# Kernel tuning notes

Measured on AMD Instinct MI355X. Metric: run time of the kernel, lower is better.

## Reference

```python
import jax, jax.numpy as jnp
import numpy as np

N = 100000      # nodes
E = 1600000     # edges (avg degree 16)
D = 64          # in_channels == conv widths == lin width
G = 64          # graphs in batch
OUT = 10        # out_channels


def setup_inputs() -> dict:
    key = jax.random.key(0)
    ks = jax.random.split(key, 20)
    s = 0.1
    inp = {
        "x": jax.random.normal(ks[0], (N, D), jnp.float32),
        "edge_index": jax.random.randint(ks[1], (2, E), 0, N, dtype=jnp.int64),
        "batch": jnp.sort(jax.random.randint(ks[2], (N,), 0, G, dtype=jnp.int64)),
    }
    k = 3
    for i in range(3):  # 3 SAGEConv layers: lin_l (Wl, bl) on aggregated, lin_r (Wr, no bias) on root
        inp[f"c{i}_Wl"] = jax.random.normal(ks[k], (D, D), jnp.float32) * s; k += 1
        inp[f"c{i}_bl"] = jnp.zeros((D,), jnp.float32)
        inp[f"c{i}_Wr"] = jax.random.normal(ks[k], (D, D), jnp.float32) * s; k += 1
    inp["l0_W"] = jax.random.normal(ks[k], (D, D), jnp.float32) * s; k += 1
    inp["l0_b"] = jnp.zeros((D,), jnp.float32)
    inp["out_W"] = jax.random.normal(ks[k], (D, OUT), jnp.float32) * s; k += 1
    inp["out_b"] = jnp.zeros((OUT,), jnp.float32)
    return inp


def reference(x, edge_index, batch,
              c0_Wl, c0_bl, c0_Wr,
              c1_Wl, c1_bl, c1_Wr,
              c2_Wl, c2_bl, c2_Wr,
              l0_W, l0_b, out_W, out_b):
    src, dst = edge_index[0], edge_index[1]
    # in-degree of each target node (mean conv aggregation), computed once
    deg = jax.ops.segment_sum(jnp.ones((E,), x.dtype), dst, num_segments=N)
    inv_deg = (1.0 / jnp.maximum(deg, 1.0))[:, None]

    def sage(h, Wl, bl, Wr):
        # gather source features, mean-aggregate at targets, then lin_l(agg) + lin_r(h)
        agg = jax.ops.segment_sum(h[src], dst, num_segments=N) * inv_deg
        return agg @ Wl + bl + h @ Wr

    h = jax.nn.relu(sage(x, c0_Wl, c0_bl, c0_Wr))
    h = jax.nn.relu(sage(h, c1_Wl, c1_bl, c1_Wr))
    h = jax.nn.relu(sage(h, c2_Wl, c2_bl, c2_Wr))

    # global mean pool over graphs
    cnt = jax.ops.segment_sum(jnp.ones((N,), h.dtype), batch, num_segments=G)
    g = jax.ops.segment_sum(h, batch, num_segments=G) / jnp.maximum(cnt, 1.0)[:, None]

    g = jax.nn.relu(g @ l0_W + l0_b)
    return g @ out_W + out_b  # [G, OUT]
```

## Files before the change

### kernel.cpp

```cpp
#include <hip/hip_runtime.h>
#include <hip/hip_fp16.h>

#define WPB 8
#define PADK 136
#define BSH 8
#define BNODES 256
#define SC_BLOCKS 256
#define HIST_BLOCKS 256

typedef _Float16 half8 __attribute__((ext_vector_type(8)));
typedef float floatx4 __attribute__((ext_vector_type(4)));

#define TS16(v) (((((v)[0] + (v)[1]) + ((v)[2] + (v)[3])) + (((v)[4] + (v)[5]) + ((v)[6] + (v)[7]))) + \
                 ((((v)[8] + (v)[9]) + ((v)[10] + (v)[11])) + (((v)[12] + (v)[13]) + ((v)[14] + (v)[15]))))

__global__ __launch_bounds__(256) void gnn_pre(const int* __restrict__ dst,
                                               int* __restrict__ bkt_cnt, int nbkt, int E,
                                               const int* __restrict__ batch,
                                               float* __restrict__ gcnt, int N,
                                               const float4* __restrict__ xin,
                                               ushort4* __restrict__ x16o, int n4,
                                               __half* __restrict__ x16,
                                               __half* __restrict__ hA,
                                               __half* __restrict__ hB) {
    int tid = threadIdx.x;
    if (blockIdx.x < HIST_BLOCKS) {
        __shared__ int h[512];
        __shared__ int gb[64];
        for (int i = tid; i < nbkt; i += 256) h[i] = 0;
        if (tid < 64) gb[tid] = 0;
        __syncthreads();
        const int stride = HIST_BLOCKS * 256;
        for (int e = blockIdx.x * 256 + tid; e < E; e += stride)
            atomicAdd(&h[dst[e] >> BSH], 1);
        for (int i = blockIdx.x * 256 + tid; i < N; i += stride)
            atomicAdd(&gb[batch[i]], 1);
        __syncthreads();
        for (int i = tid; i < nbkt; i += 256) {
            int v = h[i];
            if (v) atomicAdd(&bkt_cnt[i], v);
        }
        if (tid < 64) {
            int v = gb[tid];
            if (v) atomicAdd(&gcnt[tid], (float)v);
        }
        if (blockIdx.x == 0 && tid < 64) {
            x16[(size_t)N * 64 + tid] = __ushort_as_half((unsigned short)0);
            hA[(size_t)N * 64 + tid] = __ushort_as_half((unsigned short)0);
            hB[(size_t)N * 64 + tid] = __ushort_as_half((unsigned short)0);
        }
    } else {
        int i = (blockIdx.x - HIST_BLOCKS) * 256 + tid;
        if (i < n4) {
            float4 f = xin[i];
            ushort4 o;
            o.x = __half_as_ushort(__float2half(f.x));
            o.y = __half_as_ushort(__float2half(f.y));
            o.z = __half_as_ushort(__float2half(f.z));
            o.w = __half_as_ushort(__float2half(f.w));
            x16o[i] = o;
        }
    }
}

__global__ void gnn_bkt_scan(const int* __restrict__ bkt_cnt, int* __restrict__ bkt_base,
                             int* __restrict__ bkt_cur, int* __restrict__ row_ptr,
                             int nbkt, int N) {
    int lane = threadIdx.x;
    int carry = 0;
    for (int base = 0; base < nbkt; base += 64) {
        int idx = base + lane;
        int v = (idx < nbkt) ? bkt_cnt[idx] : 0;
        int x = v;
#pragma unroll
        for (int off = 1; off < 64; off <<= 1) {
            int y = __shfl_up(x, off);
            if (lane >= off) x += y;
        }
        if (idx < nbkt) {
            bkt_base[idx] = carry + (x - v);
            bkt_cur[idx] = carry + (x - v);
        }
        carry += __shfl(x, 63);
    }
    if (lane == 0) {
        bkt_base[nbkt] = carry;
        row_ptr[N] = carry;
    }
}

__global__ __launch_bounds__(256) void gnn_bkt_scatter(const int* __restrict__ src,
                                                       const int* __restrict__ dst,
                                                       int* __restrict__ bkt_cur,
                                                       unsigned int* __restrict__ pairs,
                                                       int E, int nbkt) {
    __shared__ int hist[512];
    __shared__ int cur[512];
    int tid = threadIdx.x;
    int chunk = (E + gridDim.x - 1) / gridDim.x;
    int e0 = blockIdx.x * chunk;
    int e1 = min(E, e0 + chunk);
    for (int i = tid; i < nbkt; i += 256) hist[i] = 0;
    __syncthreads();
    for (int e = e0 + tid; e < e1; e += 256) atomicAdd(&hist[dst[e] >> BSH], 1);
    __syncthreads();
    for (int b = tid; b < nbkt; b += 256) {
        int c = hist[b];
        cur[b] = c ? atomicAdd(&bkt_cur[b], c) : 0;
    }
    __syncthreads();
    for (int e = e0 + tid; e < e1; e += 256) {
        int d = dst[e];
        int b = d >> BSH;
        int p = atomicAdd(&cur[b], 1);
        pairs[p] = (unsigned int)src[e] | ((unsigned int)(d & (BNODES - 1)) << 24);
    }
}

__global__ __launch_bounds__(256) void gnn_bkt_csr(const unsigned int* __restrict__ pairs,
                                                   const int* __restrict__ bkt_base,
                                                   int* __restrict__ row_ptr,
                                                   float* __restrict__ inv_deg,
                                                   int* __restrict__ csr_src, int N) {
    __shared__ int hist[BNODES];
    __shared__ int excl[BNODES];
    __shared__ int cur[BNODES];
    int b = blockIdx.x;
    int base = bkt_base[b];
    int cnt = bkt_base[b + 1] - base;
    int nd0 = b << BSH;
    int tid = threadIdx.x;
    hist[tid] = 0;
    __syncthreads();
    for (int i = tid; i < cnt; i += 256) atomicAdd(&hist[pairs[base + i] >> 24], 1);
    __syncthreads();
    if (tid < 64) {
        int carry = 0;
#pragma unroll
        for (int c = 0; c < BNODES; c += 64) {
            int v = hist[c + tid];
            int x = v;
#pragma unroll
            for (int off = 1; off < 64; off <<= 1) {
                int y = __shfl_up(x, off);
                if (tid >= off) x += y;
            }
            excl[c + tid] = carry + (x - v);
            carry += __shfl(x, 63);
        }
    }
    __syncthreads();
    {
        int node = nd0 + tid;
        if (node < N) {
            row_ptr[node] = base + excl[tid];
            int d = hist[tid];
            inv_deg[node] = 1.0f / (float)(d > 1 ? d : 1);
        }
        cur[tid] = excl[tid];
    }
    __syncthreads();
    for (int i = tid; i < cnt; i += 256) {
        unsigned int u = pairs[base + i];
        int j = u >> 24;
        int pos = atomicAdd(&cur[j], 1);
        csr_src[base + pos] = (int)(u & 0xFFFFFFu);
    }
}

__global__ __launch_bounds__(512, 6) void gnn_sage(const __half* __restrict__ hin,
                                                   __half* __restrict__ hout,
                                                   const int* __restrict__ row_ptr,
                                                   const int* __restrict__ csr_src,
                                                   const float* __restrict__ inv_deg,
                                                   const float* __restrict__ Wl,
                                                   const float* __restrict__ bl,
                                                   const float* __restrict__ Wr, int n) {
    __shared__ _Float16 w_lds[64 * PADK];
    __shared__ _Float16 in_lds[WPB][16 * PADK];
    int tid = threadIdx.x, lane = tid & 63, wv = tid >> 6;
    for (int i = tid; i < 64 * 64; i += 512) {
        int k = i >> 6, nn = i & 63;
        w_lds[nn * PADK + k] = (_Float16)Wl[i];
        w_lds[nn * PADK + 64 + k] = (_Float16)Wr[i];
    }
    __syncthreads();
    int ngroups = (n + 15) >> 4;
    int g = blockIdx.x * WPB + wv;
    if (g >= ngroups) return;
    int m16 = lane & 15, quad = lane >> 4;
    float bias[4];
#pragma unroll
    for (int nt = 0; nt < 4; nt++) bias[nt] = bl[nt * 16 + m16];
    _Float16* my_in = in_lds[wv];
    const _Float16* hin16 = (const _Float16*)hin;
    int nd0 = g << 4;
    for (int j2 = 0; j2 < 16; j2 += 2) {
        int ndA = min(nd0 + j2, n - 1);
        int ndB = min(nd0 + j2 + 1, n - 1);
        int s0A = row_ptr[ndA], s1A = row_ptr[ndA + 1];
        int s0B = row_ptr[ndB], s1B = row_ptr[ndB + 1];
        float idgA = inv_deg[ndA], idgB = inv_deg[ndB];
        my_in[j2 * PADK + 64 + lane] = hin16[(size_t)ndA * 64 + lane];
        my_in[(j2 + 1) * PADK + 64 + lane] = hin16[(size_t)ndB * 64 + lane];
        float accA = 0.0f, accB = 0.0f;
        int cbA = min(64, s1A - s0A);
        int cbB = min(64, s1B - s0B);
        int eA = (lane < cbA) ? csr_src[s0A + lane] : n;
        int eB = (lane < cbB) ? csr_src[s0B + lane] : n;
#pragma unroll
        for (int ib = 0; ib < 4; ib++) {
            const int i0 = ib * 16;
            if (i0 < cbA) {
                float vA[16];
#pragma unroll
                for (int j = 0; j < 16; j++) {
                    int sj = __shfl(eA, i0 + j);
                    vA[j] = __half2float(hin[(size_t)sj * 64 + lane]);
                }
                accA += TS16(vA);
            }
            if (i0 < cbB) {
                float vB[16];
#pragma unroll
                for (int j = 0; j < 16; j++) {
                    int sj = __shfl(eB, i0 + j);
                    vB[j] = __half2float(hin[(size_t)sj * 64 + lane]);
                }
                accB += TS16(vB);
            }
        }
        for (int base = s0A + 64; base < s1A; base += 64) {
            int cb = min(64, s1A - base);
            int ei = (lane < cb) ? csr_src[base + lane] : n;
#pragma unroll
            for (int ib = 0; ib < 4; ib++) {
                const int i0 = ib * 16;
                if (i0 < cb) {
                    float v[16];
#pragma unroll
                    for (int j = 0; j < 16; j++) {
                        int s = __shfl(ei, i0 + j);
                        v[j] = __half2float(hin[(size_t)s * 64 + lane]);
                    }
                    accA += TS16(v);
                }
            }
        }
        for (int base = s0B + 64; base < s1B; base += 64) {
            int cb = min(64, s1B - base);
            int ei = (lane < cb) ? csr_src[base + lane] : n;
#pragma unroll
            for (int ib = 0; ib < 4; ib++) {
                const int i0 = ib * 16;
                if (i0 < cb) {
                    float v[16];
#pragma unroll
                    for (int j = 0; j < 16; j++) {
                        int s = __shfl(ei, i0 + j);
                        v[j] = __half2float(hin[(size_t)s * 64 + lane]);
                    }
                    accB += TS16(v);
                }
            }
        }
        my_in[j2 * PADK + lane] = (_Float16)(accA * idgA);
        my_in[(j2 + 1) * PADK + lane] = (_Float16)(accB * idgB);
    }
    half8 afrag[4];
    const _Float16* abase = my_in + m16 * PADK + quad * 8;
#pragma unroll
    for (int ks = 0; ks < 4; ks++) afrag[ks] = *(const half8*)(abase + ks * 32);
    floatx4 accv[4];
#pragma unroll
    for (int nt = 0; nt < 4; nt++) {
        accv[nt].x = 0.f; accv[nt].y = 0.f; accv[nt].z = 0.f; accv[nt].w = 0.f;
    }
#pragma unroll
    for (int nt = 0; nt < 4; nt++) {
        const _Float16* bbase = w_lds + (nt * 16 + m16) * PADK + quad * 8;
#pragma unroll
        for (int ks = 0; ks < 4; ks++) {
            half8 bfrag = *(const half8*)(bbase + ks * 32);
            accv[nt] = __builtin_amdgcn_mfma_f32_16x16x32_f16(afrag[ks], bfrag, accv[nt], 0, 0, 0);
        }
    }
#pragma unroll
    for (int nt = 0; nt < 4; nt++) {
#pragma unroll
        for (int r = 0; r < 4; r++) {
            int node = nd0 + quad * 4 + r;
            if (node < n) {
                float v = fmaxf(accv[nt][r] + bias[nt], 0.0f);
                hout[(size_t)node * 64 + nt * 16 + m16] = __float2half(v);
            }
        }
    }
}

__global__ __launch_bounds__(512, 6) void gnn_sage_pool(const __half* __restrict__ hin,
                                                        const int* __restrict__ row_ptr,
                                                        const int* __restrict__ csr_src,
                                                        const float* __restrict__ inv_deg,
                                                        const float* __restrict__ Wl,
                                                        const float* __restrict__ bl,
                                                        const float* __restrict__ Wr,
                                                        const int* __restrict__ batch,
                                                        float* __restrict__ gsum, int n) {
    __shared__ _Float16 w_lds[64 * PADK];
    __shared__ _Float16 in_lds[WPB][16 * PADK];
    int tid = threadIdx.x, lane = tid & 63, wv = tid >> 6;
    for (int i = tid; i < 64 * 64; i += 512) {
        int k = i >> 6, nn = i & 63;
        w_lds[nn * PADK + k] = (_Float16)Wl[i];
        w_lds[nn * PADK + 64 + k] = (_Float16)Wr[i];
    }
    __syncthreads();
    int ngroups = (n + 15) >> 4;
    int g = blockIdx.x * WPB + wv;
    if (g >= ngroups) return;
    int m16 = lane & 15, quad = lane >> 4;
    float bias[4];
#pragma unroll
    for (int nt = 0; nt < 4; nt++) bias[nt] = bl[nt * 16 + m16];
    _Float16* my_in = in_lds[wv];
    const _Float16* hin16 = (const _Float16*)hin;
    int nd0 = g << 4;
    for (int j2 = 0; j2 < 16; j2 += 2) {
        int ndA = min(nd0 + j2, n - 1);
        int ndB = min(nd0 + j2 + 1, n - 1);
        int s0A = row_ptr[ndA], s1A = row_ptr[ndA + 1];
        int s0B = row_ptr[ndB], s1B = row_ptr[ndB + 1];
        float idgA = inv_deg[ndA], idgB = inv_deg[ndB];
        my_in[j2 * PADK + 64 + lane] = hin16[(size_t)ndA * 64 + lane];
        my_in[(j2 + 1) * PADK + 64 + lane] = hin16[(size_t)ndB * 64 + lane];
        float accA = 0.0f, accB = 0.0f;
        int cbA = min(64, s1A - s0A);
        int cbB = min(64, s1B - s0B);
        int eA = (lane < cbA) ? csr_src[s0A + lane] : n;
        int eB = (lane < cbB) ? csr_src[s0B + lane] : n;
#pragma unroll
        for (int ib = 0; ib < 4; ib++) {
            const int i0 = ib * 16;
            if (i0 < cbA) {
                float vA[16];
#pragma unroll
                for (int j = 0; j < 16; j++) {
                    int sj = __shfl(eA, i0 + j);
                    vA[j] = __half2float(hin[(size_t)sj * 64 + lane]);
                }
                accA += TS16(vA);
            }
            if (i0 < cbB) {
                float vB[16];
#pragma unroll
                for (int j = 0; j < 16; j++) {
                    int sj = __shfl(eB, i0 + j);
                    vB[j] = __half2float(hin[(size_t)sj * 64 + lane]);
                }
                accB += TS16(vB);
            }
        }
        for (int base = s0A + 64; base < s1A; base += 64) {
            int cb = min(64, s1A - base);
            int ei = (lane < cb) ? csr_src[base + lane] : n;
#pragma unroll
            for (int ib = 0; ib < 4; ib++) {
                const int i0 = ib * 16;
                if (i0 < cb) {
                    float v[16];
#pragma unroll
                    for (int j = 0; j < 16; j++) {
                        int s = __shfl(ei, i0 + j);
                        v[j] = __half2float(hin[(size_t)s * 64 + lane]);
                    }
                    accA += TS16(v);
                }
            }
        }
        for (int base = s0B + 64; base < s1B; base += 64) {
            int cb = min(64, s1B - base);
            int ei = (lane < cb) ? csr_src[base + lane] : n;
#pragma unroll
            for (int ib = 0; ib < 4; ib++) {
                const int i0 = ib * 16;
                if (i0 < cb) {
                    float v[16];
#pragma unroll
                    for (int j = 0; j < 16; j++) {
                        int s = __shfl(ei, i0 + j);
                        v[j] = __half2float(hin[(size_t)s * 64 + lane]);
                    }
                    accB += TS16(v);
                }
            }
        }
        my_in[j2 * PADK + lane] = (_Float16)(accA * idgA);
        my_in[(j2 + 1) * PADK + lane] = (_Float16)(accB * idgB);
    }
    half8 afrag[4];
    const _Float16* abase = my_in + m16 * PADK + quad * 8;
#pragma unroll
    for (int ks = 0; ks < 4; ks++) afrag[ks] = *(const half8*)(abase + ks * 32);
    floatx4 accv[4];
#pragma unroll
    for (int nt = 0; nt < 4; nt++) {
        accv[nt].x = 0.f; accv[nt].y = 0.f; accv[nt].z = 0.f; accv[nt].w = 0.f;
    }
#pragma unroll
    for (int nt = 0; nt < 4; nt++) {
        const _Float16* bbase = w_lds + (nt * 16 + m16) * PADK + quad * 8;
#pragma unroll
        for (int ks = 0; ks < 4; ks++) {
            half8 bfrag = *(const half8*)(bbase + ks * 32);
            accv[nt] = __builtin_amdgcn_mfma_f32_16x16x32_f16(afrag[ks], bfrag, accv[nt], 0, 0, 0);
        }
    }
    int bFirst = batch[nd0];
    int bLast = batch[min(nd0 + 15, n - 1)];
    if (bFirst == bLast && nd0 + 15 < n) {
#pragma unroll
        for (int nt = 0; nt < 4; nt++) {
            float s = fmaxf(accv[nt][0] + bias[nt], 0.0f) + fmaxf(accv[nt][1] + bias[nt], 0.0f) +
                      fmaxf(accv[nt][2] + bias[nt], 0.0f) + fmaxf(accv[nt][3] + bias[nt], 0.0f);
            s += __shfl_xor(s, 16);
            s += __shfl_xor(s, 32);
            if (quad == 0) atomicAdd(&gsum[bFirst * 64 + nt * 16 + m16], s);
        }
    } else {
#pragma unroll
        for (int nt = 0; nt < 4; nt++) {
#pragma unroll
            for (int r = 0; r < 4; r++) {
                int node = nd0 + quad * 4 + r;
                if (node < n) {
                    int bg = batch[node];
                    float v = fmaxf(accv[nt][r] + bias[nt], 0.0f);
                    atomicAdd(&gsum[bg * 64 + nt * 16 + m16], v);
                }
            }
        }
    }
}

__global__ __launch_bounds__(256) void gnn_head(const float* __restrict__ gsum,
                                                const float* __restrict__ gcnt,
                                                const float* __restrict__ l0W,
                                                const float* __restrict__ l0b,
                                                const float* __restrict__ outW,
                                                const float* __restrict__ outb,
                                                float* __restrict__ out, int G, int OUT) {
    __shared__ float gm[64 * 64];
    __shared__ float t2[64 * 64];
    int tid = threadIdx.x;
    for (int i = tid; i < G * 64; i += 256) {
        int r = i >> 6;
        gm[i] = gsum[i] / fmaxf(gcnt[r], 1.0f);
    }
    __syncthreads();
    for (int i = tid; i < G * 64; i += 256) {
        int r = i >> 6, c = i & 63;
        float s = l0b[c];
#pragma unroll 8
        for (int k = 0; k < 64; k++) s += gm[(r << 6) + k] * l0W[(k << 6) + c];
        t2[i] = fmaxf(s, 0.0f);
    }
    __syncthreads();
    for (int i = tid; i < G * OUT; i += 256) {
        int r = i / OUT, c = i - r * OUT;
        float s = outb[c];
#pragma unroll 8
        for (int k = 0; k < 64; k++) s += t2[(r << 6) + k] * outW[k * OUT + c];
        out[i] = s;
    }
}

extern "C" void kernel_launch(void* const* d_in, const int* in_sizes, int n_in,
                              void* d_out, int out_size, void* d_ws, size_t ws_size,
                              hipStream_t stream) {
    const float* x = (const float*)d_in[0];
    const int* ei = (const int*)d_in[1];
    const int* batch = (const int*)d_in[2];
    const float* Wl[3] = {(const float*)d_in[3], (const float*)d_in[6], (const float*)d_in[9]};
    const float* bl[3] = {(const float*)d_in[4], (const float*)d_in[7], (const float*)d_in[10]};
    const float* Wr[3] = {(const float*)d_in[5], (const float*)d_in[8], (const float*)d_in[11]};
    const float* l0W = (const float*)d_in[12];
    const float* l0b = (const float*)d_in[13];
    const float* outW = (const float*)d_in[14];
    const float* outb = (const float*)d_in[15];

    int N = in_sizes[2];
    int E = in_sizes[1] / 2;
    int OUT = 10;
    int G = out_size / OUT;
    const int* src = ei;
    const int* dst = ei + E;
    int NBKT = (N + BNODES - 1) >> BSH;

    char* ws = (char*)d_ws;
    size_t off = 0;
    auto alloc = [&](size_t b) -> char* {
        char* p = ws + off;
        off = (off + b + 255) & ~(size_t)255;
        return p;
    };
    int* row_ptr = (int*)alloc((size_t)(N + 1) * 4);
    int* csr_src = (int*)alloc((size_t)E * 4);
    float* inv_deg = (float*)alloc((size_t)N * 4);
    size_t zoff = off;
    int* bkt_cnt = (int*)alloc((size_t)NBKT * 4);
    float* gcnt = (float*)alloc((size_t)G * 4);
    float* gsum = (float*)alloc((size_t)G * 64 * 4);
    size_t zlen = off - zoff;
    int* bkt_base = (int*)alloc((size_t)(NBKT + 1) * 4);
    int* bkt_cur = (int*)alloc((size_t)NBKT * 4);
    unsigned int* pairs = (unsigned int*)alloc((size_t)E * 4);
    __half* x16 = (__half*)alloc((size_t)(N + 1) * 64 * 2);
    __half* hA = (__half*)alloc((size_t)(N + 1) * 64 * 2);
    __half* hB = (__half*)alloc((size_t)(N + 1) * 64 * 2);

    hipMemsetAsync(ws + zoff, 0, zlen, stream);

    int n4 = N * 64 / 4;
    int pre_blocks = HIST_BLOCKS + (n4 + 255) / 256;
    gnn_pre<<<pre_blocks, 256, 0, stream>>>(dst, bkt_cnt, NBKT, E, batch, gcnt, N,
                                            (const float4*)x, (ushort4*)x16, n4,
                                            x16, hA, hB);
    gnn_bkt_scan<<<1, 64, 0, stream>>>(bkt_cnt, bkt_base, bkt_cur, row_ptr, NBKT, N);
    gnn_bkt_scatter<<<SC_BLOCKS, 256, 0, stream>>>(src, dst, bkt_cur, pairs, E, NBKT);
    gnn_bkt_csr<<<NBKT, 256, 0, stream>>>(pairs, bkt_base, row_ptr, inv_deg, csr_src, N);

    int ngroups = (N + 15) >> 4;
    int sage_blocks = (ngroups + WPB - 1) / WPB;
    gnn_sage<<<sage_blocks, 512, 0, stream>>>(x16, hA, row_ptr, csr_src, inv_deg,
                                              Wl[0], bl[0], Wr[0], N);
    gnn_sage<<<sage_blocks, 512, 0, stream>>>(hA, hB, row_ptr, csr_src, inv_deg,
                                              Wl[1], bl[1], Wr[1], N);
    gnn_sage_pool<<<sage_blocks, 512, 0, stream>>>(hB, row_ptr, csr_src, inv_deg,
                                                   Wl[2], bl[2], Wr[2], batch, gsum, N);

    gnn_head<<<1, 256, 0, stream>>>(gsum, gcnt, l0W, l0b, outW, outb, (float*)d_out, G, OUT);
}
```

Baseline: 350.8 us.

## Reuse per-block bucket histograms to skip the re-histogram pass in scatter

The pre kernel now writes each block's bucket histogram to global memory. A new scan kernel turns these into per-block, per-bucket exclusive offsets. The scatter kernel then loads those offsets directly, so it no longer re-reads dst to rebuild a histogram or takes global atomics on bucket cursors. It also switches from chunked to grid-strided edge partitioning to match the histogram blocks. This adds an extra kernel launch and about 1 MB of histogram traffic.

```diff
diff --git a/kernel.cpp b/kernel.cpp
--- a/kernel.cpp
+++ b/kernel.cpp
@@ -7,6 +7,7 @@
 #define BNODES 256
 #define SC_BLOCKS 256
 #define HIST_BLOCKS 256
+#define HSTRIDE 512
 
 typedef _Float16 half8 __attribute__((ext_vector_type(8)));
 typedef float floatx4 __attribute__((ext_vector_type(4)));
@@ -22,7 +23,8 @@
                                                ushort4* __restrict__ x16o, int n4,
                                                __half* __restrict__ x16,
                                                __half* __restrict__ hA,
-                                               __half* __restrict__ hB) {
+                                               __half* __restrict__ hB,
+                                               int* __restrict__ hist_all) {
     int tid = threadIdx.x;
     if (blockIdx.x < HIST_BLOCKS) {
         __shared__ int h[512];
@@ -38,6 +40,7 @@
         __syncthreads();
         for (int i = tid; i < nbkt; i += 256) {
             int v = h[i];
+            hist_all[blockIdx.x * HSTRIDE + i] = v;
             if (v) atomicAdd(&bkt_cnt[i], v);
         }
         if (tid < 64) {
@@ -64,8 +67,7 @@
 }
 
 __global__ void gnn_bkt_scan(const int* __restrict__ bkt_cnt, int* __restrict__ bkt_base,
-                             int* __restrict__ bkt_cur, int* __restrict__ row_ptr,
-                             int nbkt, int N) {
+                             int* __restrict__ row_ptr, int nbkt, int N) {
     int lane = threadIdx.x;
     int carry = 0;
     for (int base = 0; base < nbkt; base += 64) {
@@ -77,10 +79,7 @@
             int y = __shfl_up(x, off);
             if (lane >= off) x += y;
         }
-        if (idx < nbkt) {
-            bkt_base[idx] = carry + (x - v);
-            bkt_cur[idx] = carry + (x - v);
-        }
+        if (idx < nbkt) bkt_base[idx] = carry + (x - v);
         carry += __shfl(x, 63);
     }
     if (lane == 0) {
@@ -89,27 +88,37 @@
     }
 }
 
+__global__ __launch_bounds__(256) void gnn_scan2(const int* __restrict__ hist_all,
+                                                 const int* __restrict__ bkt_base,
+                                                 int* __restrict__ blk_base_all, int nbkt) {
+    int b = blockIdx.x;
+    int t = threadIdx.x, lane = t & 63, wv = t >> 6;
+    __shared__ int wsum[4];
+    int v = hist_all[t * HSTRIDE + b];
+    int x = v;
+#pragma unroll
+    for (int off = 1; off < 64; off <<= 1) {
+        int y = __shfl_up(x, off);
+        if (lane >= off) x += y;
+    }
+    if (lane == 63) wsum[wv] = x;
+    __syncthreads();
+    int wexcl = 0;
+    for (int w = 0; w < wv; w++) wexcl += wsum[w];
+    blk_base_all[t * HSTRIDE + b] = bkt_base[b] + wexcl + (x - v);
+}
+
 __global__ __launch_bounds__(256) void gnn_bkt_scatter(const int* __restrict__ src,
                                                        const int* __restrict__ dst,
-                                                       int* __restrict__ bkt_cur,
+                                                       const int* __restrict__ blk_base_all,
                                                        unsigned int* __restrict__ pairs,
                                                        int E, int nbkt) {
-    __shared__ int hist[512];
     __shared__ int cur[512];
     int tid = threadIdx.x;
-    int chunk = (E + gridDim.x - 1) / gridDim.x;
-    int e0 = blockIdx.x * chunk;
-    int e1 = min(E, e0 + chunk);
-    for (int i = tid; i < nbkt; i += 256) hist[i] = 0;
-    __syncthreads();
-    for (int e = e0 + tid; e < e1; e += 256) atomicAdd(&hist[dst[e] >> BSH], 1);
-    __syncthreads();
-    for (int b = tid; b < nbkt; b += 256) {
-        int c = hist[b];
-        cur[b] = c ? atomicAdd(&bkt_cur[b], c) : 0;
-    }
-    __syncthreads();
-    for (int e = e0 + tid; e < e1; e += 256) {
+    for (int i = tid; i < nbkt; i += 256) cur[i] = blk_base_all[blockIdx.x * HSTRIDE + i];
+    __syncthreads();
+    const int stride = SC_BLOCKS * 256;
+    for (int e = blockIdx.x * 256 + tid; e < E; e += stride) {
         int d = dst[e];
         int b = d >> BSH;
         int p = atomicAdd(&cur[b], 1);
@@ -513,7 +522,8 @@
     float* gsum = (float*)alloc((size_t)G * 64 * 4);
     size_t zlen = off - zoff;
     int* bkt_base = (int*)alloc((size_t)(NBKT + 1) * 4);
-    int* bkt_cur = (int*)alloc((size_t)NBKT * 4);
+    int* hist_all = (int*)alloc((size_t)HIST_BLOCKS * HSTRIDE * 4);
+    int* blk_base_all = (int*)alloc((size_t)HIST_BLOCKS * HSTRIDE * 4);
     unsigned int* pairs = (unsigned int*)alloc((size_t)E * 4);
     __half* x16 = (__half*)alloc((size_t)(N + 1) * 64 * 2);
     __half* hA = (__half*)alloc((size_t)(N + 1) * 64 * 2);
@@ -525,9 +535,10 @@
     int pre_blocks = HIST_BLOCKS + (n4 + 255) / 256;
     gnn_pre<<<pre_blocks, 256, 0, stream>>>(dst, bkt_cnt, NBKT, E, batch, gcnt, N,
                                             (const float4*)x, (ushort4*)x16, n4,
-                                            x16, hA, hB);
-    gnn_bkt_scan<<<1, 64, 0, stream>>>(bkt_cnt, bkt_base, bkt_cur, row_ptr, NBKT, N);
-    gnn_bkt_scatter<<<SC_BLOCKS, 256, 0, stream>>>(src, dst, bkt_cur, pairs, E, NBKT);
+                                            x16, hA, hB, hist_all);
+    gnn_bkt_scan<<<1, 64, 0, stream>>>(bkt_cnt, bkt_base, row_ptr, NBKT, N);
+    gnn_scan2<<<NBKT, 256, 0, stream>>>(hist_all, bkt_base, blk_base_all, NBKT);
+    gnn_bkt_scatter<<<SC_BLOCKS, 256, 0, stream>>>(src, dst, blk_base_all, pairs, E, NBKT);
     gnn_bkt_csr<<<NBKT, 256, 0, stream>>>(pairs, bkt_base, row_ptr, inv_deg, csr_src, N);
 
     int ngroups = (N + 15) >> 4;
```

Result: no change. 345.3 us (-1.6%).
